# Optimization experiments

Measured on AMD Instinct MI355X. Metric: run time of the kernel, lower is better.

## Reference

```python
import jax, jax.numpy as jnp
import numpy as np

WINDOW = 5  # window_size from init


def _avg_pool3d(x, k):
    # Matches F.avg_pool3d(kernel=k, stride=1, padding=k//2,
    # count_include_pad=True): windowed sum with zero padding / k^3.
    pad = k // 2
    s = jax.lax.reduce_window(
        x, 0.0, jax.lax.add,
        window_dimensions=(1, 1, k, k, k),
        window_strides=(1, 1, 1, 1, 1),
        padding=[(0, 0), (0, 0), (pad, pad), (pad, pad), (pad, pad)],
    )
    return s / float(k ** 3)


def setup_inputs() -> dict:
    key = jax.random.key(0)
    k1, k2 = jax.random.split(key)
    shape = (2, 1, 160, 192, 192)  # [B, C, D, H, W]
    source = jax.random.normal(k1, shape, dtype=jnp.float32)
    target = jax.random.normal(k2, shape, dtype=jnp.float32)
    return {"source": source, "target": target}


def reference(source, target):
    conv = lambda x: _avg_pool3d(x, WINDOW)
    src_mean = conv(source)
    tgt_mean = conv(target)
    src_var = conv(source * source) - src_mean * src_mean
    tgt_var = conv(target * target) - tgt_mean * tgt_mean
    cross = conv(source * target) - src_mean * tgt_mean
    lncc = cross * cross / (src_var * tgt_var + 1e-5)
    loss = 1.0 - jnp.mean(lncc)
    return jnp.nan_to_num(loss, nan=1.0, posinf=1.0, neginf=1.0)
```

## Files before the change

### kernel.cpp

```cpp
#include <hip/hip_runtime.h>
#include <math.h>

#define W_ 192
#define H_ 192
#define D_ 160
#define B_ 2
#define XT 32
#define YT 16
#define HY 20
#define CHUNK 10
#define PLANES (CHUNK + 4)
#define GXD 6
#define GYD 12
#define GZD 32
#define NBLK (GXD * GYD * GZD)
#define NTOT 11796480.0f

__device__ __forceinline__ float2 f2add(float2 u, float2 v) { return make_float2(u.x + v.x, u.y + v.y); }
__device__ __forceinline__ float2 f2sub(float2 u, float2 v) { return make_float2(u.x - v.x, u.y - v.y); }

__global__ __launch_bounds__(256) void lncc_main(const float* __restrict__ src,
                                                 const float* __restrict__ tgt,
                                                 float* __restrict__ partial) {
    __shared__ float4 raw[HY][19];
    __shared__ float2 rsS [HY][17];
    __shared__ float2 rsT [HY][17];
    __shared__ float2 rsS2[HY][17];
    __shared__ float2 rsT2[HY][17];
    __shared__ float2 rsST[HY][17];
    __shared__ float wsum[4];

    const int tx  = threadIdx.x, ty = threadIdx.y;
    const int tid = ty * 16 + tx;
    const int bz  = blockIdx.z;
    const int b   = bz >> 4;
    const int z0  = (bz & 15) * CHUNK;
    const int bx0 = blockIdx.x * XT - 2;
    const int by0 = blockIdx.y * YT - 2;

    const int  r0s = tid / 18,          c0s = tid - r0s * 18;
    const int  s1  = 256 + tid;
    const int  r1s = s1 / 18,           c1s = s1 - r1s * 18;
    const bool has2 = (tid < 104);

    auto load_slot = [&](int r, int c, int zp, float2& vS, float2& vT) {
        vS = make_float2(0.f, 0.f); vT = make_float2(0.f, 0.f);
        const int gx = bx0 + 2 * c, gy = by0 + r;
        if ((unsigned)zp < (unsigned)D_ && (unsigned)gy < (unsigned)H_ &&
            (unsigned)gx < (unsigned)W_) {
            const size_t off = (size_t)(b * D_ + zp) * (size_t)(H_ * W_)
                             + (size_t)gy * W_ + (size_t)gx;
            vS = *(const float2*)(src + off);
            vT = *(const float2*)(tgt + off);
        }
    };
    auto store_slot = [&](int r, int c, float2 vS, float2 vT) {
        raw[r][c] = make_float4(vS.x, vT.x, vS.y, vT.y);
    };

    auto do_pair = [&](int p) {
        const int r = p >> 4, px = p & 15;
        float4 A  = raw[r][px];
        float4 Bv = raw[r][px + 1];
        float4 C  = raw[r][px + 2];
        float s0 = A.x,  t0 = A.y,  sx1 = A.z,  tx1 = A.w;
        float s2 = Bv.x, t2 = Bv.y, s3 = Bv.z,  t3 = Bv.w;
        float s4 = C.x,  t4 = C.y,  s5 = C.z,   t5 = C.w;
        float S0 = s0 + sx1 + s2 + s3 + s4;
        float T0 = t0 + tx1 + t2 + t3 + t4;
        float A0 = fmaf(s4, s4, fmaf(s3, s3, fmaf(s2, s2, fmaf(sx1, sx1, s0 * s0))));
        float B0 = fmaf(t4, t4, fmaf(t3, t3, fmaf(t2, t2, fmaf(tx1, tx1, t0 * t0))));
        float C0 = fmaf(s4, t4, fmaf(s3, t3, fmaf(s2, t2, fmaf(sx1, tx1, s0 * t0))));
        float S1 = S0 - s0 + s5;
        float T1 = T0 - t0 + t5;
        float A1 = fmaf(s5, s5, fmaf(-s0, s0, A0));
        float B1 = fmaf(t5, t5, fmaf(-t0, t0, B0));
        float C1 = fmaf(s5, t5, fmaf(-s0, t0, C0));
        rsS [r][px] = make_float2(S0, S1);
        rsT [r][px] = make_float2(T0, T1);
        rsS2[r][px] = make_float2(A0, A1);
        rsT2[r][px] = make_float2(B0, B1);
        rsST[r][px] = make_float2(C0, C1);
    };

    float2 q0s={0,0},q0t={0,0},q0a={0,0},q0b={0,0},q0c={0,0};
    float2 q1s={0,0},q1t={0,0},q1a={0,0},q1b={0,0},q1c={0,0};
    float2 q2s={0,0},q2t={0,0},q2a={0,0},q2b={0,0},q2c={0,0};
    float2 q3s={0,0},q3t={0,0},q3a={0,0},q3b={0,0},q3c={0,0};
    float2 q4s={0,0},q4t={0,0},q4a={0,0},q4b={0,0},q4c={0,0};
    float2 zS={0,0},zT={0,0},zA={0,0},zB={0,0},zC={0,0};
    float2 lsum = make_float2(0.f, 0.f);

    {
        float2 aS, aT, bS, bT;
        load_slot(r0s, c0s, z0 - 2, aS, aT);
        if (has2) load_slot(r1s, c1s, z0 - 2, bS, bT);
        store_slot(r0s, c0s, aS, aT);
        if (has2) store_slot(r1s, c1s, bS, bT);
    }

    for (int i = 0; i < PLANES; ++i) {
        __syncthreads();
        float2 aS, aT, bS, bT;
        const bool haveNext = (i + 1 < PLANES);
        if (haveNext) {
            load_slot(r0s, c0s, z0 - 1 + i, aS, aT);
            if (has2) load_slot(r1s, c1s, z0 - 1 + i, bS, bT);
        }
        do_pair(tid);
        if (tid < 64) do_pair(256 + tid);
        __syncthreads();
        if (haveNext) {
            store_slot(r0s, c0s, aS, aT);
            if (has2) store_slot(r1s, c1s, bS, bT);
        }
        {
            float2 yS = make_float2(0.f, 0.f), yT = yS, yA = yS, yB = yS, yC = yS;
            #pragma unroll
            for (int dy = 0; dy < 5; ++dy) {
                yS = f2add(yS, rsS [ty + dy][tx]);
                yT = f2add(yT, rsT [ty + dy][tx]);
                yA = f2add(yA, rsS2[ty + dy][tx]);
                yB = f2add(yB, rsT2[ty + dy][tx]);
                yC = f2add(yC, rsST[ty + dy][tx]);
            }
            zS = f2add(zS, f2sub(yS, q0s));
            zT = f2add(zT, f2sub(yT, q0t));
            zA = f2add(zA, f2sub(yA, q0a));
            zB = f2add(zB, f2sub(yB, q0b));
            zC = f2add(zC, f2sub(yC, q0c));
            q0s=q1s; q0t=q1t; q0a=q1a; q0b=q1b; q0c=q1c;
            q1s=q2s; q1t=q2t; q1a=q2a; q1b=q2b; q1c=q2c;
            q2s=q3s; q2t=q3t; q2a=q3a; q2b=q3b; q2c=q3c;
            q3s=q4s; q3t=q4t; q3a=q4a; q3b=q4b; q3c=q4c;
            q4s=yS;  q4t=yT;  q4a=yA;  q4b=yB;  q4c=yC;
            if (i >= 4) {
                const float inv = 1.0f / 125.0f;
                {
                    float ms = zS.x * inv, mt = zT.x * inv;
                    float vs = fmaf(-ms, ms, zA.x * inv);
                    float vt = fmaf(-mt, mt, zB.x * inv);
                    float cr = fmaf(-ms, mt, zC.x * inv);
                    float den = fmaf(vs, vt, 1e-5f);
                    lsum.x = fmaf(cr * cr, __builtin_amdgcn_rcpf(den), lsum.x);
                }
                {
                    float ms = zS.y * inv, mt = zT.y * inv;
                    float vs = fmaf(-ms, ms, zA.y * inv);
                    float vt = fmaf(-mt, mt, zB.y * inv);
                    float cr = fmaf(-ms, mt, zC.y * inv);
                    float den = fmaf(vs, vt, 1e-5f);
                    lsum.y = fmaf(cr * cr, __builtin_amdgcn_rcpf(den), lsum.y);
                }
            }
        }
    }

    float ls = lsum.x + lsum.y;
    #pragma unroll
    for (int off = 32; off > 0; off >>= 1)
        ls += __shfl_down(ls, off, 64);
    if ((tid & 63) == 0) wsum[tid >> 6] = ls;
    __syncthreads();
    if (tid == 0) {
        const int bid = (blockIdx.z * GYD + blockIdx.y) * GXD + blockIdx.x;
        partial[bid] = wsum[0] + wsum[1] + wsum[2] + wsum[3];
    }
}

__global__ __launch_bounds__(256) void lncc_finalize(const float* __restrict__ partial,
                                                     float* __restrict__ out) {
    __shared__ float ws[4];
    const int t = threadIdx.x;
    float s = 0.0f;
    for (int i = t; i < NBLK; i += 256) s += partial[i];
    #pragma unroll
    for (int off = 32; off > 0; off >>= 1) s += __shfl_down(s, off, 64);
    if ((t & 63) == 0) ws[t >> 6] = s;
    __syncthreads();
    if (t == 0) {
        float tot = ws[0] + ws[1] + ws[2] + ws[3];
        float loss = 1.0f - tot * (1.0f / NTOT);
        if (isnan(loss) || isinf(loss)) loss = 1.0f;
        *out = loss;
    }
}

extern "C" void kernel_launch(void* const* d_in, const int* in_sizes, int n_in,
                              void* d_out, int out_size, void* d_ws, size_t ws_size,
                              hipStream_t stream) {
    const float* src = (const float*)d_in[0];
    const float* tgt = (const float*)d_in[1];
    float* out = (float*)d_out;
    float* partial = (float*)d_ws;

    dim3 grid(GXD, GYD, GZD);
    dim3 block(16, 16, 1);
    lncc_main<<<grid, block, 0, stream>>>(src, tgt, partial);
    lncc_finalize<<<dim3(1), dim3(256), 0, stream>>>(partial, out);
}
```

Measured before the change: 175.4 us.

## Widen x tile to 64 and swap separable pass order with 4 outputs per thread

Doubles the block's x tile to 64 columns, so each thread now produces four adjacent x outputs instead of two. The in-plane box sum now runs the y direction first: 136 threads each slide a 5-row window over a column of pairs. The x direction then uses a sliding window over float2 column sums to form four outputs. The aim is to cut the halo overhead per output and the shared-memory reads per output, and to amortise the z-ring bookkeeping over more outputs. In exchange each thread holds more registers (float4 rings, with launch bounds set to 3 blocks per CU), only about half the threads take part in the column pass, and the grid has half as many blocks.

```diff
diff --git a/kernel.cpp b/kernel.cpp
--- a/kernel.cpp
+++ b/kernel.cpp
@@ -5,43 +5,56 @@
 #define H_ 192
 #define D_ 160
 #define B_ 2
-#define XT 32
+#define XT 64
 #define YT 16
+#define XP 34
 #define HY 20
 #define CHUNK 10
 #define PLANES (CHUNK + 4)
-#define GXD 6
+#define GXD 3
 #define GYD 12
 #define GZD 32
 #define NBLK (GXD * GYD * GZD)
+#define CSP 35
 #define NTOT 11796480.0f
 
-__device__ __forceinline__ float2 f2add(float2 u, float2 v) { return make_float2(u.x + v.x, u.y + v.y); }
-__device__ __forceinline__ float2 f2sub(float2 u, float2 v) { return make_float2(u.x - v.x, u.y - v.y); }
-
-__global__ __launch_bounds__(256) void lncc_main(const float* __restrict__ src,
-                                                 const float* __restrict__ tgt,
-                                                 float* __restrict__ partial) {
-    __shared__ float4 raw[HY][19];
-    __shared__ float2 rsS [HY][17];
-    __shared__ float2 rsT [HY][17];
-    __shared__ float2 rsS2[HY][17];
-    __shared__ float2 rsT2[HY][17];
-    __shared__ float2 rsST[HY][17];
+__device__ __forceinline__ float4 f4add(float4 a, float4 b) {
+    return make_float4(a.x + b.x, a.y + b.y, a.z + b.z, a.w + b.w);
+}
+__device__ __forceinline__ float4 f4sub(float4 a, float4 b) {
+    return make_float4(a.x - b.x, a.y - b.y, a.z - b.z, a.w - b.w);
+}
+__device__ __forceinline__ float4 win8(float2 a, float2 b, float2 c, float2 d) {
+    float W0 = a.x + a.y + b.x + b.y + c.x;
+    float W1 = W0 + (c.y - a.x);
+    float W2 = W1 + (d.x - a.y);
+    float W3 = W2 + (d.y - b.x);
+    return make_float4(W0, W1, W2, W3);
+}
+
+__global__ __launch_bounds__(256, 3) void lncc_main(const float* __restrict__ src,
+                                                    const float* __restrict__ tgt,
+                                                    float* __restrict__ partial) {
+    __shared__ float4 raw[HY][XP];
+    __shared__ float2 csS[YT][CSP], csT[YT][CSP],
+                      csA[YT][CSP], csB[YT][CSP], csC[YT][CSP];
     __shared__ float wsum[4];
 
-    const int tx  = threadIdx.x, ty = threadIdx.y;
-    const int tid = ty * 16 + tx;
+    const int tid = threadIdx.x;
+    const int xg  = tid & 15;
+    const int ty  = tid >> 4;
     const int bz  = blockIdx.z;
     const int b   = bz >> 4;
     const int z0  = (bz & 15) * CHUNK;
     const int bx0 = blockIdx.x * XT - 2;
     const int by0 = blockIdx.y * YT - 2;
 
-    const int  r0s = tid / 18,          c0s = tid - r0s * 18;
-    const int  s1  = 256 + tid;
-    const int  r1s = s1 / 18,           c1s = s1 - r1s * 18;
-    const bool has2 = (tid < 104);
+    const int  sA_r = tid / 34,         sA_c = tid - sA_r * 34;
+    const int  sB   = tid + 256;
+    const int  sB_r = sB / 34,          sB_c = sB - sB_r * 34;
+    const int  sC   = tid + 512;
+    const int  sC_r = sC / 34,          sC_c = sC - sC_r * 34;
+    const bool has3 = (tid < 168);
 
     auto load_slot = [&](int r, int c, int zp, float2& vS, float2& vT) {
         vS = make_float2(0.f, 0.f); vT = make_float2(0.f, 0.f);
@@ -58,105 +71,127 @@
         raw[r][c] = make_float4(vS.x, vT.x, vS.y, vT.y);
     };
 
-    auto do_pair = [&](int p) {
-        const int r = p >> 4, px = p & 15;
-        float4 A  = raw[r][px];
-        float4 Bv = raw[r][px + 1];
-        float4 C  = raw[r][px + 2];
-        float s0 = A.x,  t0 = A.y,  sx1 = A.z,  tx1 = A.w;
-        float s2 = Bv.x, t2 = Bv.y, s3 = Bv.z,  t3 = Bv.w;
-        float s4 = C.x,  t4 = C.y,  s5 = C.z,   t5 = C.w;
-        float S0 = s0 + sx1 + s2 + s3 + s4;
-        float T0 = t0 + tx1 + t2 + t3 + t4;
-        float A0 = fmaf(s4, s4, fmaf(s3, s3, fmaf(s2, s2, fmaf(sx1, sx1, s0 * s0))));
-        float B0 = fmaf(t4, t4, fmaf(t3, t3, fmaf(t2, t2, fmaf(tx1, tx1, t0 * t0))));
-        float C0 = fmaf(s4, t4, fmaf(s3, t3, fmaf(s2, t2, fmaf(sx1, tx1, s0 * t0))));
-        float S1 = S0 - s0 + s5;
-        float T1 = T0 - t0 + t5;
-        float A1 = fmaf(s5, s5, fmaf(-s0, s0, A0));
-        float B1 = fmaf(t5, t5, fmaf(-t0, t0, B0));
-        float C1 = fmaf(s5, t5, fmaf(-s0, t0, C0));
-        rsS [r][px] = make_float2(S0, S1);
-        rsT [r][px] = make_float2(T0, T1);
-        rsS2[r][px] = make_float2(A0, A1);
-        rsT2[r][px] = make_float2(B0, B1);
-        rsST[r][px] = make_float2(C0, C1);
-    };
-
-    float2 q0s={0,0},q0t={0,0},q0a={0,0},q0b={0,0},q0c={0,0};
-    float2 q1s={0,0},q1t={0,0},q1a={0,0},q1b={0,0},q1c={0,0};
-    float2 q2s={0,0},q2t={0,0},q2a={0,0},q2b={0,0},q2c={0,0};
-    float2 q3s={0,0},q3t={0,0},q3a={0,0},q3b={0,0},q3c={0,0};
-    float2 q4s={0,0},q4t={0,0},q4a={0,0},q4b={0,0},q4c={0,0};
-    float2 zS={0,0},zT={0,0},zA={0,0},zB={0,0},zC={0,0};
-    float2 lsum = make_float2(0.f, 0.f);
+    const bool p1act = (tid < 136);
+    const int  p1p   = tid % 34;
+    const int  p1g   = tid / 34;
+
+    float4 q0S={0,0,0,0},q0T={0,0,0,0},q0A={0,0,0,0},q0B={0,0,0,0},q0C={0,0,0,0};
+    float4 q1S={0,0,0,0},q1T={0,0,0,0},q1A={0,0,0,0},q1B={0,0,0,0},q1C={0,0,0,0};
+    float4 q2S={0,0,0,0},q2T={0,0,0,0},q2A={0,0,0,0},q2B={0,0,0,0},q2C={0,0,0,0};
+    float4 q3S={0,0,0,0},q3T={0,0,0,0},q3A={0,0,0,0},q3B={0,0,0,0},q3C={0,0,0,0};
+    float4 q4S={0,0,0,0},q4T={0,0,0,0},q4A={0,0,0,0},q4B={0,0,0,0},q4C={0,0,0,0};
+    float4 zS={0,0,0,0},zT={0,0,0,0},zA={0,0,0,0},zB={0,0,0,0},zC={0,0,0,0};
+    float4 lsum = {0,0,0,0};
 
     {
-        float2 aS, aT, bS, bT;
-        load_slot(r0s, c0s, z0 - 2, aS, aT);
-        if (has2) load_slot(r1s, c1s, z0 - 2, bS, bT);
-        store_slot(r0s, c0s, aS, aT);
-        if (has2) store_slot(r1s, c1s, bS, bT);
+        float2 aS, aT, bS, bT, cS, cT;
+        load_slot(sA_r, sA_c, z0 - 2, aS, aT);
+        load_slot(sB_r, sB_c, z0 - 2, bS, bT);
+        if (has3) load_slot(sC_r, sC_c, z0 - 2, cS, cT);
+        store_slot(sA_r, sA_c, aS, aT);
+        store_slot(sB_r, sB_c, bS, bT);
+        if (has3) store_slot(sC_r, sC_c, cS, cT);
     }
 
     for (int i = 0; i < PLANES; ++i) {
         __syncthreads();
-        float2 aS, aT, bS, bT;
+        float2 aS, aT, bS, bT, cS, cT;
         const bool haveNext = (i + 1 < PLANES);
         if (haveNext) {
-            load_slot(r0s, c0s, z0 - 1 + i, aS, aT);
-            if (has2) load_slot(r1s, c1s, z0 - 1 + i, bS, bT);
-        }
-        do_pair(tid);
-        if (tid < 64) do_pair(256 + tid);
+            const int zpn = z0 - 1 + i;
+            load_slot(sA_r, sA_c, zpn, aS, aT);
+            load_slot(sB_r, sB_c, zpn, bS, bT);
+            if (has3) load_slot(sC_r, sC_c, zpn, cS, cT);
+        }
+        if (p1act) {
+            const int p = p1p, y0g = p1g * 4;
+            float4 r0 = raw[y0g + 0][p];
+            float4 r1 = raw[y0g + 1][p];
+            float4 r2 = raw[y0g + 2][p];
+            float4 r3 = raw[y0g + 3][p];
+            float4 r4 = raw[y0g + 4][p];
+            float S0 = r0.x + r1.x + r2.x + r3.x + r4.x;
+            float S1 = r0.z + r1.z + r2.z + r3.z + r4.z;
+            float T0 = r0.y + r1.y + r2.y + r3.y + r4.y;
+            float T1 = r0.w + r1.w + r2.w + r3.w + r4.w;
+            float A0 = fmaf(r4.x, r4.x, fmaf(r3.x, r3.x, fmaf(r2.x, r2.x, fmaf(r1.x, r1.x, r0.x * r0.x))));
+            float A1 = fmaf(r4.z, r4.z, fmaf(r3.z, r3.z, fmaf(r2.z, r2.z, fmaf(r1.z, r1.z, r0.z * r0.z))));
+            float B0 = fmaf(r4.y, r4.y, fmaf(r3.y, r3.y, fmaf(r2.y, r2.y, fmaf(r1.y, r1.y, r0.y * r0.y))));
+            float B1 = fmaf(r4.w, r4.w, fmaf(r3.w, r3.w, fmaf(r2.w, r2.w, fmaf(r1.w, r1.w, r0.w * r0.w))));
+            float C0 = fmaf(r4.x, r4.y, fmaf(r3.x, r3.y, fmaf(r2.x, r2.y, fmaf(r1.x, r1.y, r0.x * r0.y))));
+            float C1 = fmaf(r4.z, r4.w, fmaf(r3.z, r3.w, fmaf(r2.z, r2.w, fmaf(r1.z, r1.w, r0.z * r0.w))));
+            csS[y0g][p] = make_float2(S0, S1);
+            csT[y0g][p] = make_float2(T0, T1);
+            csA[y0g][p] = make_float2(A0, A1);
+            csB[y0g][p] = make_float2(B0, B1);
+            csC[y0g][p] = make_float2(C0, C1);
+            #pragma unroll
+            for (int m = 1; m <= 3; ++m) {
+                float4 rn = raw[y0g + 4 + m][p];
+                S0 += rn.x - r0.x;  S1 += rn.z - r0.z;
+                T0 += rn.y - r0.y;  T1 += rn.w - r0.w;
+                A0 = fmaf(rn.x, rn.x, fmaf(-r0.x, r0.x, A0));
+                A1 = fmaf(rn.z, rn.z, fmaf(-r0.z, r0.z, A1));
+                B0 = fmaf(rn.y, rn.y, fmaf(-r0.y, r0.y, B0));
+                B1 = fmaf(rn.w, rn.w, fmaf(-r0.w, r0.w, B1));
+                C0 = fmaf(rn.x, rn.y, fmaf(-r0.x, r0.y, C0));
+                C1 = fmaf(rn.z, rn.w, fmaf(-r0.z, r0.w, C1));
+                r0 = r1; r1 = r2; r2 = r3; r3 = r4; r4 = rn;
+                csS[y0g + m][p] = make_float2(S0, S1);
+                csT[y0g + m][p] = make_float2(T0, T1);
+                csA[y0g + m][p] = make_float2(A0, A1);
+                csB[y0g + m][p] = make_float2(B0, B1);
+                csC[y0g + m][p] = make_float2(C0, C1);
+            }
+        }
         __syncthreads();
         if (haveNext) {
-            store_slot(r0s, c0s, aS, aT);
-            if (has2) store_slot(r1s, c1s, bS, bT);
+            store_slot(sA_r, sA_c, aS, aT);
+            store_slot(sB_r, sB_c, bS, bT);
+            if (has3) store_slot(sC_r, sC_c, cS, cT);
         }
         {
-            float2 yS = make_float2(0.f, 0.f), yT = yS, yA = yS, yB = yS, yC = yS;
-            #pragma unroll
-            for (int dy = 0; dy < 5; ++dy) {
-                yS = f2add(yS, rsS [ty + dy][tx]);
-                yT = f2add(yT, rsT [ty + dy][tx]);
-                yA = f2add(yA, rsS2[ty + dy][tx]);
-                yB = f2add(yB, rsT2[ty + dy][tx]);
-                yC = f2add(yC, rsST[ty + dy][tx]);
-            }
-            zS = f2add(zS, f2sub(yS, q0s));
-            zT = f2add(zT, f2sub(yT, q0t));
-            zA = f2add(zA, f2sub(yA, q0a));
-            zB = f2add(zB, f2sub(yB, q0b));
-            zC = f2add(zC, f2sub(yC, q0c));
-            q0s=q1s; q0t=q1t; q0a=q1a; q0b=q1b; q0c=q1c;
-            q1s=q2s; q1t=q2t; q1a=q2a; q1b=q2b; q1c=q2c;
-            q2s=q3s; q2t=q3t; q2a=q3a; q2b=q3b; q2c=q3c;
-            q3s=q4s; q3t=q4t; q3a=q4a; q3b=q4b; q3c=q4c;
-            q4s=yS;  q4t=yT;  q4a=yA;  q4b=yB;  q4c=yC;
+            const int p2 = 2 * xg;
+            float4 ysS, ysT, ysA, ysB, ysC;
+            { float2 a = csS[ty][p2], b2 = csS[ty][p2+1], c2 = csS[ty][p2+2], d = csS[ty][p2+3];
+              ysS = win8(a, b2, c2, d); }
+            { float2 a = csT[ty][p2], b2 = csT[ty][p2+1], c2 = csT[ty][p2+2], d = csT[ty][p2+3];
+              ysT = win8(a, b2, c2, d); }
+            { float2 a = csA[ty][p2], b2 = csA[ty][p2+1], c2 = csA[ty][p2+2], d = csA[ty][p2+3];
+              ysA = win8(a, b2, c2, d); }
+            { float2 a = csB[ty][p2], b2 = csB[ty][p2+1], c2 = csB[ty][p2+2], d = csB[ty][p2+3];
+              ysB = win8(a, b2, c2, d); }
+            { float2 a = csC[ty][p2], b2 = csC[ty][p2+1], c2 = csC[ty][p2+2], d = csC[ty][p2+3];
+              ysC = win8(a, b2, c2, d); }
+            zS = f4add(zS, f4sub(ysS, q0S));
+            zT = f4add(zT, f4sub(ysT, q0T));
+            zA = f4add(zA, f4sub(ysA, q0A));
+            zB = f4add(zB, f4sub(ysB, q0B));
+            zC = f4add(zC, f4sub(ysC, q0C));
+            q0S=q1S; q0T=q1T; q0A=q1A; q0B=q1B; q0C=q1C;
+            q1S=q2S; q1T=q2T; q1A=q2A; q1B=q2B; q1C=q2C;
+            q2S=q3S; q2T=q3T; q2A=q3A; q2B=q3B; q2C=q3C;
+            q3S=q4S; q3T=q4T; q3A=q4A; q3B=q4B; q3C=q4C;
+            q4S=ysS; q4T=ysT; q4A=ysA; q4B=ysB; q4C=ysC;
             if (i >= 4) {
                 const float inv = 1.0f / 125.0f;
-                {
-                    float ms = zS.x * inv, mt = zT.x * inv;
-                    float vs = fmaf(-ms, ms, zA.x * inv);
-                    float vt = fmaf(-mt, mt, zB.x * inv);
-                    float cr = fmaf(-ms, mt, zC.x * inv);
+                auto accum = [&](float s, float t, float a2, float b2, float c2, float& acc) {
+                    float ms = s * inv, mt = t * inv;
+                    float vs = fmaf(-ms, ms, a2 * inv);
+                    float vt = fmaf(-mt, mt, b2 * inv);
+                    float cr = fmaf(-ms, mt, c2 * inv);
                     float den = fmaf(vs, vt, 1e-5f);
-                    lsum.x = fmaf(cr * cr, __builtin_amdgcn_rcpf(den), lsum.x);
-                }
-                {
-                    float ms = zS.y * inv, mt = zT.y * inv;
-                    float vs = fmaf(-ms, ms, zA.y * inv);
-                    float vt = fmaf(-mt, mt, zB.y * inv);
-                    float cr = fmaf(-ms, mt, zC.y * inv);
-                    float den = fmaf(vs, vt, 1e-5f);
-                    lsum.y = fmaf(cr * cr, __builtin_amdgcn_rcpf(den), lsum.y);
-                }
+                    acc = fmaf(cr * cr, __builtin_amdgcn_rcpf(den), acc);
+                };
+                accum(zS.x, zT.x, zA.x, zB.x, zC.x, lsum.x);
+                accum(zS.y, zT.y, zA.y, zB.y, zC.y, lsum.y);
+                accum(zS.z, zT.z, zA.z, zB.z, zC.z, lsum.z);
+                accum(zS.w, zT.w, zA.w, zB.w, zC.w, lsum.w);
             }
         }
     }
 
-    float ls = lsum.x + lsum.y;
+    float ls = (lsum.x + lsum.y) + (lsum.z + lsum.w);
     #pragma unroll
     for (int off = 32; off > 0; off >>= 1)
         ls += __shfl_down(ls, off, 64);
@@ -195,7 +230,7 @@
     float* partial = (float*)d_ws;
 
     dim3 grid(GXD, GYD, GZD);
-    dim3 block(16, 16, 1);
+    dim3 block(256, 1, 1);
     lncc_main<<<grid, block, 0, stream>>>(src, tgt, partial);
     lncc_finalize<<<dim3(1), dim3(256), 0, stream>>>(partial, out);
 }
```

After: 272.2 us. +55.2%, slower.

## Reorder box filter to column-first sliding sums and double z-chunk per block

Applied to the files above, without the earlier changes.

The per-plane separable sum now runs vertically first. 72 threads each compute a running 5-row sum over 4 output rows, so row sums are reused through a sliding window instead of being recomputed. The horizontal 5-tap sum then reads from the packed even/odd column arrays. The z chunk per block doubles from 10 to 20 planes, which halves the redundant 4-plane halo loads but also halves the grid, lowering parallelism. Phase 1 now uses only 72 of 256 threads, which risks load imbalance and a serial critical path between the barriers.

```diff
diff --git a/kernel.cpp b/kernel.cpp
--- a/kernel.cpp
+++ b/kernel.cpp
@@ -8,11 +8,12 @@
 #define XT 32
 #define YT 16
 #define HY 20
-#define CHUNK 10
+#define NPAIR 18
+#define CHUNK 20
 #define PLANES (CHUNK + 4)
 #define GXD 6
 #define GYD 12
-#define GZD 32
+#define GZD 16
 #define NBLK (GXD * GYD * GZD)
 #define NTOT 11796480.0f
 
@@ -22,25 +23,23 @@
 __global__ __launch_bounds__(256) void lncc_main(const float* __restrict__ src,
                                                  const float* __restrict__ tgt,
                                                  float* __restrict__ partial) {
-    __shared__ float4 raw[HY][19];
-    __shared__ float2 rsS [HY][17];
-    __shared__ float2 rsT [HY][17];
-    __shared__ float2 rsS2[HY][17];
-    __shared__ float2 rsT2[HY][17];
-    __shared__ float2 rsST[HY][17];
+    __shared__ float4 raw[HY][NPAIR + 1];
+    __shared__ float4 csQ[YT][2 * NPAIR + 1];
+    __shared__ float2 csC[YT][NPAIR + 1];
     __shared__ float wsum[4];
 
-    const int tx  = threadIdx.x, ty = threadIdx.y;
-    const int tid = ty * 16 + tx;
+    const int tid = threadIdx.x;
+    const int tx  = tid & 15;
+    const int ty  = tid >> 4;
     const int bz  = blockIdx.z;
-    const int b   = bz >> 4;
-    const int z0  = (bz & 15) * CHUNK;
+    const int b   = bz >> 3;
+    const int z0  = (bz & 7) * CHUNK;
     const int bx0 = blockIdx.x * XT - 2;
     const int by0 = blockIdx.y * YT - 2;
 
-    const int  r0s = tid / 18,          c0s = tid - r0s * 18;
-    const int  s1  = 256 + tid;
-    const int  r1s = s1 / 18,           c1s = s1 - r1s * 18;
+    const int  sA_r = tid / 18,  sA_c = tid - sA_r * 18;
+    const int  sB   = tid + 256;
+    const int  sB_r = sB / 18,   sB_c = sB - sB_r * 18;
     const bool has2 = (tid < 104);
 
     auto load_slot = [&](int r, int c, int zp, float2& vS, float2& vT) {
@@ -58,45 +57,24 @@
         raw[r][c] = make_float4(vS.x, vT.x, vS.y, vT.y);
     };
 
-    auto do_pair = [&](int p) {
-        const int r = p >> 4, px = p & 15;
-        float4 A  = raw[r][px];
-        float4 Bv = raw[r][px + 1];
-        float4 C  = raw[r][px + 2];
-        float s0 = A.x,  t0 = A.y,  sx1 = A.z,  tx1 = A.w;
-        float s2 = Bv.x, t2 = Bv.y, s3 = Bv.z,  t3 = Bv.w;
-        float s4 = C.x,  t4 = C.y,  s5 = C.z,   t5 = C.w;
-        float S0 = s0 + sx1 + s2 + s3 + s4;
-        float T0 = t0 + tx1 + t2 + t3 + t4;
-        float A0 = fmaf(s4, s4, fmaf(s3, s3, fmaf(s2, s2, fmaf(sx1, sx1, s0 * s0))));
-        float B0 = fmaf(t4, t4, fmaf(t3, t3, fmaf(t2, t2, fmaf(tx1, tx1, t0 * t0))));
-        float C0 = fmaf(s4, t4, fmaf(s3, t3, fmaf(s2, t2, fmaf(sx1, tx1, s0 * t0))));
-        float S1 = S0 - s0 + s5;
-        float T1 = T0 - t0 + t5;
-        float A1 = fmaf(s5, s5, fmaf(-s0, s0, A0));
-        float B1 = fmaf(t5, t5, fmaf(-t0, t0, B0));
-        float C1 = fmaf(s5, t5, fmaf(-s0, t0, C0));
-        rsS [r][px] = make_float2(S0, S1);
-        rsT [r][px] = make_float2(T0, T1);
-        rsS2[r][px] = make_float2(A0, A1);
-        rsT2[r][px] = make_float2(B0, B1);
-        rsST[r][px] = make_float2(C0, C1);
-    };
-
-    float2 q0s={0,0},q0t={0,0},q0a={0,0},q0b={0,0},q0c={0,0};
-    float2 q1s={0,0},q1t={0,0},q1a={0,0},q1b={0,0},q1c={0,0};
-    float2 q2s={0,0},q2t={0,0},q2a={0,0},q2b={0,0},q2c={0,0};
-    float2 q3s={0,0},q3t={0,0},q3a={0,0},q3b={0,0},q3c={0,0};
-    float2 q4s={0,0},q4t={0,0},q4a={0,0},q4b={0,0},q4c={0,0};
+    const bool p1act = (tid < 72);
+    const int  p1p   = tid % 18;
+    const int  p1g   = tid / 18;
+
+    float2 q0S={0,0},q0T={0,0},q0A={0,0},q0B={0,0},q0C={0,0};
+    float2 q1S={0,0},q1T={0,0},q1A={0,0},q1B={0,0},q1C={0,0};
+    float2 q2S={0,0},q2T={0,0},q2A={0,0},q2B={0,0},q2C={0,0};
+    float2 q3S={0,0},q3T={0,0},q3A={0,0},q3B={0,0},q3C={0,0};
+    float2 q4S={0,0},q4T={0,0},q4A={0,0},q4B={0,0},q4C={0,0};
     float2 zS={0,0},zT={0,0},zA={0,0},zB={0,0},zC={0,0};
     float2 lsum = make_float2(0.f, 0.f);
 
     {
         float2 aS, aT, bS, bT;
-        load_slot(r0s, c0s, z0 - 2, aS, aT);
-        if (has2) load_slot(r1s, c1s, z0 - 2, bS, bT);
-        store_slot(r0s, c0s, aS, aT);
-        if (has2) store_slot(r1s, c1s, bS, bT);
+        load_slot(sA_r, sA_c, z0 - 2, aS, aT);
+        if (has2) load_slot(sB_r, sB_c, z0 - 2, bS, bT);
+        store_slot(sA_r, sA_c, aS, aT);
+        if (has2) store_slot(sB_r, sB_c, bS, bT);
     }
 
     for (int i = 0; i < PLANES; ++i) {
@@ -104,36 +82,78 @@
         float2 aS, aT, bS, bT;
         const bool haveNext = (i + 1 < PLANES);
         if (haveNext) {
-            load_slot(r0s, c0s, z0 - 1 + i, aS, aT);
-            if (has2) load_slot(r1s, c1s, z0 - 1 + i, bS, bT);
-        }
-        do_pair(tid);
-        if (tid < 64) do_pair(256 + tid);
+            const int zpn = z0 - 1 + i;
+            load_slot(sA_r, sA_c, zpn, aS, aT);
+            if (has2) load_slot(sB_r, sB_c, zpn, bS, bT);
+        }
+        if (p1act) {
+            const int p = p1p, y0g = p1g * 4;
+            float4 r0 = raw[y0g + 0][p];
+            float4 r1 = raw[y0g + 1][p];
+            float4 r2 = raw[y0g + 2][p];
+            float4 r3 = raw[y0g + 3][p];
+            float4 r4 = raw[y0g + 4][p];
+            float S0 = r0.x + r1.x + r2.x + r3.x + r4.x;
+            float T0 = r0.y + r1.y + r2.y + r3.y + r4.y;
+            float S1 = r0.z + r1.z + r2.z + r3.z + r4.z;
+            float T1 = r0.w + r1.w + r2.w + r3.w + r4.w;
+            float A0 = fmaf(r4.x, r4.x, fmaf(r3.x, r3.x, fmaf(r2.x, r2.x, fmaf(r1.x, r1.x, r0.x * r0.x))));
+            float B0 = fmaf(r4.y, r4.y, fmaf(r3.y, r3.y, fmaf(r2.y, r2.y, fmaf(r1.y, r1.y, r0.y * r0.y))));
+            float A1 = fmaf(r4.z, r4.z, fmaf(r3.z, r3.z, fmaf(r2.z, r2.z, fmaf(r1.z, r1.z, r0.z * r0.z))));
+            float B1 = fmaf(r4.w, r4.w, fmaf(r3.w, r3.w, fmaf(r2.w, r2.w, fmaf(r1.w, r1.w, r0.w * r0.w))));
+            float C0 = fmaf(r4.x, r4.y, fmaf(r3.x, r3.y, fmaf(r2.x, r2.y, fmaf(r1.x, r1.y, r0.x * r0.y))));
+            float C1 = fmaf(r4.z, r4.w, fmaf(r3.z, r3.w, fmaf(r2.z, r2.w, fmaf(r1.z, r1.w, r0.z * r0.w))));
+            csQ[y0g][p]          = make_float4(S0, T0, A0, B0);
+            csQ[y0g][18 + p]     = make_float4(S1, T1, A1, B1);
+            csC[y0g][p]          = make_float2(C0, C1);
+            #pragma unroll
+            for (int m = 1; m <= 3; ++m) {
+                float4 rn = raw[y0g + 4 + m][p];
+                S0 += rn.x - r0.x;  T0 += rn.y - r0.y;
+                S1 += rn.z - r0.z;  T1 += rn.w - r0.w;
+                A0 = fmaf(rn.x, rn.x, fmaf(-r0.x, r0.x, A0));
+                B0 = fmaf(rn.y, rn.y, fmaf(-r0.y, r0.y, B0));
+                A1 = fmaf(rn.z, rn.z, fmaf(-r0.z, r0.z, A1));
+                B1 = fmaf(rn.w, rn.w, fmaf(-r0.w, r0.w, B1));
+                C0 = fmaf(rn.x, rn.y, fmaf(-r0.x, r0.y, C0));
+                C1 = fmaf(rn.z, rn.w, fmaf(-r0.z, r0.w, C1));
+                r0 = r1; r1 = r2; r2 = r3; r3 = r4; r4 = rn;
+                csQ[y0g + m][p]      = make_float4(S0, T0, A0, B0);
+                csQ[y0g + m][18 + p] = make_float4(S1, T1, A1, B1);
+                csC[y0g + m][p]      = make_float2(C0, C1);
+            }
+        }
         __syncthreads();
         if (haveNext) {
-            store_slot(r0s, c0s, aS, aT);
-            if (has2) store_slot(r1s, c1s, bS, bT);
+            store_slot(sA_r, sA_c, aS, aT);
+            if (has2) store_slot(sB_r, sB_c, bS, bT);
         }
         {
-            float2 yS = make_float2(0.f, 0.f), yT = yS, yA = yS, yB = yS, yC = yS;
-            #pragma unroll
-            for (int dy = 0; dy < 5; ++dy) {
-                yS = f2add(yS, rsS [ty + dy][tx]);
-                yT = f2add(yT, rsT [ty + dy][tx]);
-                yA = f2add(yA, rsS2[ty + dy][tx]);
-                yB = f2add(yB, rsT2[ty + dy][tx]);
-                yC = f2add(yC, rsST[ty + dy][tx]);
-            }
-            zS = f2add(zS, f2sub(yS, q0s));
-            zT = f2add(zT, f2sub(yT, q0t));
-            zA = f2add(zA, f2sub(yA, q0a));
-            zB = f2add(zB, f2sub(yB, q0b));
-            zC = f2add(zC, f2sub(yC, q0c));
-            q0s=q1s; q0t=q1t; q0a=q1a; q0b=q1b; q0c=q1c;
-            q1s=q2s; q1t=q2t; q1a=q2a; q1b=q2b; q1c=q2c;
-            q2s=q3s; q2t=q3t; q2a=q3a; q2b=q3b; q2c=q3c;
-            q3s=q4s; q3t=q4t; q3a=q4a; q3b=q4b; q3c=q4c;
-            q4s=yS;  q4t=yT;  q4a=yA;  q4b=yB;  q4c=yC;
+            float4 E0 = csQ[ty][tx];
+            float4 E1 = csQ[ty][tx + 1];
+            float4 E2 = csQ[ty][tx + 2];
+            float4 O0 = csQ[ty][18 + tx];
+            float4 O1 = csQ[ty][18 + tx + 1];
+            float4 O2 = csQ[ty][18 + tx + 2];
+            float2 cc0 = csC[ty][tx];
+            float2 cc1 = csC[ty][tx + 1];
+            float2 cc2 = csC[ty][tx + 2];
+            float2 ysS, ysT, ysA, ysB, ysC;
+            { float w0 = E0.x + O0.x + E1.x + O1.x + E2.x; ysS = make_float2(w0, w0 - E0.x + O2.x); }
+            { float w0 = E0.y + O0.y + E1.y + O1.y + E2.y; ysT = make_float2(w0, w0 - E0.y + O2.y); }
+            { float w0 = E0.z + O0.z + E1.z + O1.z + E2.z; ysA = make_float2(w0, w0 - E0.z + O2.z); }
+            { float w0 = E0.w + O0.w + E1.w + O1.w + E2.w; ysB = make_float2(w0, w0 - E0.w + O2.w); }
+            { float w0 = cc0.x + cc0.y + cc1.x + cc1.y + cc2.x; ysC = make_float2(w0, w0 - cc0.x + cc2.y); }
+            zS = f2add(zS, f2sub(ysS, q0S));
+            zT = f2add(zT, f2sub(ysT, q0T));
+            zA = f2add(zA, f2sub(ysA, q0A));
+            zB = f2add(zB, f2sub(ysB, q0B));
+            zC = f2add(zC, f2sub(ysC, q0C));
+            q0S=q1S; q0T=q1T; q0A=q1A; q0B=q1B; q0C=q1C;
+            q1S=q2S; q1T=q2T; q1A=q2A; q1B=q2B; q1C=q2C;
+            q2S=q3S; q2T=q3T; q2A=q3A; q2B=q3B; q2C=q3C;
+            q3S=q4S; q3T=q4T; q3A=q4A; q3B=q4B; q3C=q4C;
+            q4S=ysS; q4T=ysT; q4A=ysA; q4B=ysB; q4C=ysC;
             if (i >= 4) {
                 const float inv = 1.0f / 125.0f;
                 {
@@ -195,7 +215,7 @@
     float* partial = (float*)d_ws;
 
     dim3 grid(GXD, GYD, GZD);
-    dim3 block(16, 16, 1);
+    dim3 block(256, 1, 1);
     lncc_main<<<grid, block, 0, stream>>>(src, tgt, partial);
     lncc_finalize<<<dim3(1), dim3(256), 0, stream>>>(partial, out);
 }
```

New measurement: 201.7 us. 15.0% more time.
